# Kernel optimization log

Measured on AMD Instinct MI355X. Metric: run time of the kernel, lower is better.

## Reference

```python
import jax, jax.numpy as jnp
import numpy as np

DIM = 64  # number of flow dimensions (block count)


def _masks(out_f, in_f, dim):
    # mask_d: 1 on the dim diagonal blocks; mask_o: 1 strictly below-block (lower-triangular off-diagonal)
    opd, ipd = out_f // dim, in_f // dim
    mask_d = np.zeros((out_f, in_f), np.float32)
    mask_o = np.ones((out_f, in_f), np.float32)
    for i in range(dim):
        mask_d[i * opd:(i + 1) * opd, i * ipd:(i + 1) * ipd] = 1.0
        mask_o[i * opd:(i + 1) * opd, i * ipd:] = 0.0
    return jnp.asarray(mask_d), jnp.asarray(mask_o)


def setup_inputs() -> dict:
    key = jax.random.key(0)
    k1, k2, k3, k4, k5 = jax.random.split(key, 5)
    B, F = 1024, 2048
    inputs = jax.random.normal(k1, (B, F), jnp.float32)
    # log-diagonal Jacobian blocks from a previous layer with per-dim input size 1
    grad = jax.random.normal(k2, (B, DIM, F // DIM, 1), jnp.float32)
    weight = jax.random.normal(k3, (F, F), jnp.float32) * 0.05
    diag_weight = jnp.log(jax.random.uniform(k4, (F, 1), jnp.float32, 1e-3, 1.0))
    bias = jax.random.uniform(k5, (F,), jnp.float32, -1.0, 1.0) / jnp.sqrt(jnp.float32(F))
    return {"inputs": inputs, "grad": grad, "weight": weight,
            "diag_weight": diag_weight, "bias": bias}


def reference(inputs, grad, weight, diag_weight, bias):
    out_f, in_f = weight.shape
    dim = DIM
    opd, ipd = out_f // dim, in_f // dim
    mask_d, mask_o = _masks(out_f, in_f, dim)

    # weight normalization with positive diagonal blocks
    w = jnp.exp(weight) * mask_d + weight * mask_o              # (out, in)
    wsn = jnp.sum(w * w, axis=-1, keepdims=True)                # (out, 1)
    w_n = jnp.exp(diag_weight) * w / jnp.sqrt(wsn)              # (out, in)
    wpl = diag_weight + weight - 0.5 * jnp.log(wsn)             # (out, in)

    out = inputs @ w_n.T + bias                                 # (B, out)

    # diagonal blocks of wpl, already transposed per-block: (dim, opd, ipd)
    wpl4 = wpl.reshape(dim, opd, dim, ipd)
    blocks = wpl4[jnp.arange(dim), :, jnp.arange(dim), :]

    B = inputs.shape[0]
    g = jnp.broadcast_to(blocks[None], (B, dim, opd, ipd))

    # combine with previous log-Jacobian: logsumexp over contracted axis
    grad_t = jnp.swapaxes(grad, -1, -2)                         # (B, dim, p, ipd)
    logdet = jax.nn.logsumexp(g[:, :, :, None, :] + grad_t[:, :, None, :, :], axis=-1)  # (B, dim, opd, p)
    return (out, logdet)
```

## Files before the change

kernel.cpp:

```cpp
#include <hip/hip_runtime.h>

#define F 2048
#define BATCH 1024

typedef short bf16x8 __attribute__((ext_vector_type(8)));
typedef float f32x4 __attribute__((ext_vector_type(4)));
typedef unsigned short u16x4 __attribute__((ext_vector_type(4)));

__device__ __forceinline__ unsigned short f2bf(float f) {
  unsigned u = __builtin_bit_cast(unsigned, f);
  unsigned r = (u + 0x7fffu + ((u >> 16) & 1u)) >> 16;
  return (unsigned short)r;
}

__device__ __forceinline__ void gload_lds16(const void* g, void* l) {
  __builtin_amdgcn_global_load_lds(
      (const __attribute__((address_space(1))) unsigned int*)g,
      (__attribute__((address_space(3))) unsigned int*)l,
      16, 0, 0);
}

__global__ __launch_bounds__(256) void prep_convert_kernel(
    const float* __restrict__ inputs, unsigned short* __restrict__ a_bf,
    const float* __restrict__ weight, const float* __restrict__ dw,
    unsigned short* __restrict__ w_n, float* __restrict__ exp_blocks)
{
  int bid = blockIdx.x;
  if (bid < 1024) {
    int idx = bid * 2048 + threadIdx.x * 8;
    float4 v0 = *(const float4*)(inputs + idx);
    float4 v1 = *(const float4*)(inputs + idx + 4);
    union { unsigned short s[8]; bf16x8 v; } o;
    o.s[0] = f2bf(v0.x); o.s[1] = f2bf(v0.y); o.s[2] = f2bf(v0.z); o.s[3] = f2bf(v0.w);
    o.s[4] = f2bf(v1.x); o.s[5] = f2bf(v1.y); o.s[6] = f2bf(v1.z); o.s[7] = f2bf(v1.w);
    *(bf16x8*)(a_bf + idx) = o.v;
    return;
  }
  int rb = bid - 1024;
  int lane = threadIdx.x & 63;
  int r = rb * 4 + (threadIdx.x >> 6);
  int i = r >> 5;
  int lim = (i + 1) * 32;
  int wlim = (r & ~63) + 64;
  int d0 = i * 32;
  const float* wrow = weight + (size_t)r * F;

  float ss = 0.f;
  for (int j = lane; j < lim / 4; j += 64) {
    float4 v = ((const float4*)wrow)[j];
    if (j * 4 >= d0) {
      v.x = __expf(v.x); v.y = __expf(v.y); v.z = __expf(v.z); v.w = __expf(v.w);
    }
    ss += v.x * v.x + v.y * v.y + v.z * v.z + v.w * v.w;
  }
#pragma unroll
  for (int d = 32; d > 0; d >>= 1) ss += __shfl_xor(ss, d, 64);

  float dwr = dw[r];
  float scale = __expf(dwr) * rsqrtf(ss);
  float halflog = 0.5f * __logf(ss);

  unsigned short* onrow = w_n + (size_t)r * F;
  for (int j = lane; j < wlim / 4; j += 64) {
    u16x4 o = {0, 0, 0, 0};
    if (j * 4 < lim) {
      float4 v = ((const float4*)wrow)[j];
      if (j * 4 >= d0) {
        v.x = __expf(v.x); v.y = __expf(v.y); v.z = __expf(v.z); v.w = __expf(v.w);
      }
      o[0] = f2bf(scale * v.x); o[1] = f2bf(scale * v.y);
      o[2] = f2bf(scale * v.z); o[3] = f2bf(scale * v.w);
    }
    *(u16x4*)(onrow + j * 4) = o;
  }
  if (lane < 32) {
    exp_blocks[(size_t)r * 32 + lane] = __expf(dwr + wrow[d0 + lane] - halflog);
  }
}

__global__ __launch_bounds__(256) void gemm_kernel(
    const unsigned short* __restrict__ A, const unsigned short* __restrict__ W,
    const float* __restrict__ bias, float* __restrict__ out)
{
  __shared__ char smem[3][2][8192];

  int id = blockIdx.x;
  int tm = id >> 5;
  int tn_raw = id & 31;
  int tn = (tm & 8) ? (31 - tn_raw) : tn_raw;
  int m0 = tm * 64, n0 = tn * 64;
  int nkt = tn + 1;

  int tid = threadIdx.x;
  int lane = tid & 63, wid = tid >> 6;
  int wm = wid >> 1, wn = wid & 1;
  int l15 = lane & 15, lg = lane >> 4;

  int srow = lane >> 3;
  int schunk = (lane & 7) ^ (srow & 7);

  auto stage = [&](int buf, int kt) {
    size_t kb = (size_t)kt * 128;
#pragma unroll
    for (int e = 0; e < 2; ++e) {
      int s = wid * 2 + e;
      int row = s * 8 + srow;
      const char* ga = (const char*)A + (size_t)(m0 + row) * (F * 2) + kb + schunk * 16;
      gload_lds16(ga, &smem[buf][0][s * 1024]);
      const char* gb = (const char*)W + (size_t)(n0 + row) * (F * 2) + kb + schunk * 16;
      gload_lds16(gb, &smem[buf][1][s * 1024]);
    }
  };

  f32x4 acc[2][2] = {};

  auto compute = [&](int buf) {
    const char* sA = smem[buf][0];
    const char* sB = smem[buf][1];
    bf16x8 af[2][2], bfr[2][2];
#pragma unroll
    for (int mi = 0; mi < 2; ++mi)
#pragma unroll
      for (int ks = 0; ks < 2; ++ks) {
        int row = wm * 32 + mi * 16 + l15;
        int ch = (ks * 4 + lg) ^ (l15 & 7);
        af[mi][ks] = *(const bf16x8*)(sA + row * 128 + ch * 16);
      }
#pragma unroll
    for (int ni = 0; ni < 2; ++ni)
#pragma unroll
      for (int ks = 0; ks < 2; ++ks) {
        int row = wn * 32 + ni * 16 + l15;
        int ch = (ks * 4 + lg) ^ (l15 & 7);
        bfr[ni][ks] = *(const bf16x8*)(sB + row * 128 + ch * 16);
      }
#pragma unroll
    for (int ks = 0; ks < 2; ++ks)
#pragma unroll
      for (int mi = 0; mi < 2; ++mi)
#pragma unroll
        for (int ni = 0; ni < 2; ++ni)
          acc[mi][ni] = __builtin_amdgcn_mfma_f32_16x16x32_bf16(
              af[mi][ks], bfr[ni][ks], acc[mi][ni], 0, 0, 0);
  };

  stage(0, 0);
  if (nkt > 1) stage(1, 1);
  for (int kt = 0; kt < nkt; ++kt) {
    if (kt + 2 < nkt) stage((kt + 2) % 3, kt + 2);
    int rem = nkt - 1 - kt;
    if (rem >= 2)      asm volatile("s_waitcnt vmcnt(8)" ::: "memory");
    else if (rem == 1) asm volatile("s_waitcnt vmcnt(4)" ::: "memory");
    else               asm volatile("s_waitcnt vmcnt(0)" ::: "memory");
    __builtin_amdgcn_s_barrier();
    compute(kt % 3);
    __builtin_amdgcn_s_barrier();
  }

  float bv0 = bias[n0 + wn * 32 + l15];
  float bv1 = bias[n0 + wn * 32 + 16 + l15];
#pragma unroll
  for (int mi = 0; mi < 2; ++mi)
#pragma unroll
    for (int ni = 0; ni < 2; ++ni) {
      float bv = ni ? bv1 : bv0;
#pragma unroll
      for (int j = 0; j < 4; ++j) {
        int m = m0 + wm * 32 + mi * 16 + lg * 4 + j;
        int n = n0 + wn * 32 + ni * 16 + l15;
        out[(size_t)m * F + n] = acc[mi][ni][j] + bv;
      }
    }
}

__global__ __launch_bounds__(256) void logdet_kernel(
    const float* __restrict__ grad, const float* __restrict__ exp_blocks,
    float* __restrict__ ld)
{
  __shared__ float eb[32][33];
  __shared__ float eg[32][32];
  int i = blockIdx.x & 63;
  int b0 = (blockIdx.x >> 6) * 32;
  int tid = threadIdx.x;
  int p = tid & 31, row8 = tid >> 5;

#pragma unroll
  for (int k = 0; k < 4; ++k) {
    int t = tid + k * 256;
    eb[t >> 5][t & 31] = exp_blocks[(size_t)i * 1024 + t];
  }
#pragma unroll
  for (int k = 0; k < 4; ++k) {
    int b = b0 + row8 + 8 * k;
    eg[row8 + 8 * k][p] = __expf(grad[((size_t)b * 64 + i) * 32 + p]);
  }
  __syncthreads();

  int o = p;
  float s[4] = {0.f, 0.f, 0.f, 0.f};
#pragma unroll
  for (int q = 0; q < 32; ++q) {
    float e = eb[o][q];
#pragma unroll
    for (int k = 0; k < 4; ++k) s[k] += e * eg[row8 + 8 * k][q];
  }
#pragma unroll
  for (int k = 0; k < 4; ++k) {
    int b = b0 + row8 + 8 * k;
    ld[((size_t)b * 64 + i) * 32 + o] = __logf(s[k]);
  }
}

extern "C" void kernel_launch(void* const* d_in, const int* in_sizes, int n_in,
                              void* d_out, int out_size, void* d_ws, size_t ws_size,
                              hipStream_t stream)
{
  const float* inputs = (const float*)d_in[0];
  const float* grad   = (const float*)d_in[1];
  const float* weight = (const float*)d_in[2];
  const float* dw     = (const float*)d_in[3];
  const float* bias   = (const float*)d_in[4];

  float* out = (float*)d_out;
  float* ld  = out + (size_t)BATCH * F;

  unsigned short* w_n  = (unsigned short*)d_ws;
  unsigned short* a_bf = w_n + (size_t)F * F;
  float* exp_blocks    = (float*)(a_bf + (size_t)BATCH * F);

  prep_convert_kernel<<<1536, 256, 0, stream>>>(inputs, a_bf, weight, dw, w_n, exp_blocks);
  gemm_kernel<<<512, 256, 0, stream>>>(a_bf, w_n, bias, out);
  logdet_kernel<<<64 * 32, 256, 0, stream>>>(grad, exp_blocks, ld);
}
```

Measured before the change: 106.6 us.

## Fuse logdet computation into GEMM kernel tail to drop a launch

```diff
diff --git a/kernel.cpp b/kernel.cpp
--- a/kernel.cpp
+++ b/kernel.cpp
@@ -78,11 +78,13 @@
   }
 }
 
-__global__ __launch_bounds__(256) void gemm_kernel(
+__global__ __launch_bounds__(256) void gemm_logdet_kernel(
     const unsigned short* __restrict__ A, const unsigned short* __restrict__ W,
-    const float* __restrict__ bias, float* __restrict__ out)
+    const float* __restrict__ bias, const float* __restrict__ grad,
+    const float* __restrict__ exp_blocks, float* __restrict__ out,
+    float* __restrict__ ld)
 {
-  __shared__ char smem[3][2][8192];
+  __shared__ __align__(16) char smem[3 * 16384];
 
   int id = blockIdx.x;
   int tm = id >> 5;
@@ -101,22 +103,23 @@
 
   auto stage = [&](int buf, int kt) {
     size_t kb = (size_t)kt * 128;
+    char* base = smem + buf * 16384;
 #pragma unroll
     for (int e = 0; e < 2; ++e) {
       int s = wid * 2 + e;
       int row = s * 8 + srow;
       const char* ga = (const char*)A + (size_t)(m0 + row) * (F * 2) + kb + schunk * 16;
-      gload_lds16(ga, &smem[buf][0][s * 1024]);
+      gload_lds16(ga, base + s * 1024);
       const char* gb = (const char*)W + (size_t)(n0 + row) * (F * 2) + kb + schunk * 16;
-      gload_lds16(gb, &smem[buf][1][s * 1024]);
+      gload_lds16(gb, base + 8192 + s * 1024);
     }
   };
 
   f32x4 acc[2][2] = {};
 
   auto compute = [&](int buf) {
-    const char* sA = smem[buf][0];
-    const char* sB = smem[buf][1];
+    const char* sA = smem + buf * 16384;
+    const char* sB = sA + 8192;
     bf16x8 af[2][2], bfr[2][2];
 #pragma unroll
     for (int mi = 0; mi < 2; ++mi)
@@ -171,43 +174,44 @@
         out[(size_t)m * F + n] = acc[mi][ni][j] + bv;
       }
     }
-}
-
-__global__ __launch_bounds__(256) void logdet_kernel(
-    const float* __restrict__ grad, const float* __restrict__ exp_blocks,
-    float* __restrict__ ld)
-{
-  __shared__ float eb[32][33];
-  __shared__ float eg[32][32];
-  int i = blockIdx.x & 63;
-  int b0 = (blockIdx.x >> 6) * 32;
-  int tid = threadIdx.x;
+
+  float* eb = (float*)smem;
+  float* eg = (float*)(smem + 32 * 36 * 4);
+  int li = id & 63;
+  int bg0 = (id >> 6) * 4;
   int p = tid & 31, row8 = tid >> 5;
 
 #pragma unroll
   for (int k = 0; k < 4; ++k) {
     int t = tid + k * 256;
-    eb[t >> 5][t & 31] = exp_blocks[(size_t)i * 1024 + t];
-  }
-#pragma unroll
-  for (int k = 0; k < 4; ++k) {
-    int b = b0 + row8 + 8 * k;
-    eg[row8 + 8 * k][p] = __expf(grad[((size_t)b * 64 + i) * 32 + p]);
-  }
-  __syncthreads();
-
-  int o = p;
-  float s[4] = {0.f, 0.f, 0.f, 0.f};
-#pragma unroll
-  for (int q = 0; q < 32; ++q) {
-    float e = eb[o][q];
-#pragma unroll
-    for (int k = 0; k < 4; ++k) s[k] += e * eg[row8 + 8 * k][q];
-  }
-#pragma unroll
-  for (int k = 0; k < 4; ++k) {
-    int b = b0 + row8 + 8 * k;
-    ld[((size_t)b * 64 + i) * 32 + o] = __logf(s[k]);
+    eb[(t >> 5) * 36 + (t & 31)] = exp_blocks[(size_t)li * 1024 + t];
+  }
+
+#pragma unroll
+  for (int g4 = 0; g4 < 4; ++g4) {
+    int b0 = (bg0 + g4) * 32;
+    __syncthreads();
+#pragma unroll
+    for (int k = 0; k < 4; ++k) {
+      int b = b0 + row8 + 8 * k;
+      eg[(row8 + 8 * k) * 32 + p] = __expf(grad[((size_t)b * 64 + li) * 32 + p]);
+    }
+    __syncthreads();
+    float s[4] = {0.f, 0.f, 0.f, 0.f};
+#pragma unroll
+    for (int q4 = 0; q4 < 8; ++q4) {
+      f32x4 e = *(const f32x4*)(eb + p * 36 + q4 * 4);
+#pragma unroll
+      for (int k = 0; k < 4; ++k) {
+        f32x4 g = *(const f32x4*)(eg + (row8 + 8 * k) * 32 + q4 * 4);
+        s[k] += e[0] * g[0] + e[1] * g[1] + e[2] * g[2] + e[3] * g[3];
+      }
+    }
+#pragma unroll
+    for (int k = 0; k < 4; ++k) {
+      int b = b0 + row8 + 8 * k;
+      ld[((size_t)b * 64 + li) * 32 + p] = __logf(s[k]);
+    }
   }
 }
 
@@ -229,6 +233,5 @@
   float* exp_blocks    = (float*)(a_bf + (size_t)BATCH * F);
 
   prep_convert_kernel<<<1536, 256, 0, stream>>>(inputs, a_bf, weight, dw, w_n, exp_blocks);
-  gemm_kernel<<<512, 256, 0, stream>>>(a_bf, w_n, bias, out);
-  logdet_kernel<<<64 * 32, 256, 0, stream>>>(grad, exp_blocks, ld);
-}
+  gemm_logdet_kernel<<<512, 256, 0, stream>>>(a_bf, w_n, bias, grad, exp_blocks, out, ld);
+}
```

After: 106.0 us. About the same (-0.6%).
